# Performance work log

Measured on AMD Instinct MI355X. Metric: run time of the kernel, lower is better.

## Reference

```python
import jax, jax.numpy as jnp
import numpy as np

N_CHANNELS = 22
N_PATCHES = 64
N_NODES = N_CHANNELS * N_PATCHES  # 1408
EMBED_DIM = 256
N_HEADS = 4
HEAD_DIM = EMBED_DIM // N_HEADS
ALPHA = 0.15
TOP_P = 0.85
DIST_THRESH = 0.55
BATCH = 16

TCP_PAIRS = [('FP1','F7'),('F7','T3'),('T3','T5'),('T5','O1'),('FP2','F8'),('F8','T4'),('T4','T6'),('T6','O2'),('FP1','F3'),('F3','C3'),('C3','P3'),('P3','O1'),('FP2','F4'),('F4','C4'),('C4','P4'),('P4','O2'),('A1','T3'),('T3','C3'),('C3','CZ'),('CZ','C4'),('C4','T4'),('T4','A2')]
_ELECTRODE_3D = {'FP1':(-0.31,0.95,0.0),'FP2':(0.31,0.95,0.0),'F7':(-0.81,0.59,0.0),'F3':(-0.55,0.67,0.5),'FZ':(0.0,0.71,0.71),'F4':(0.55,0.67,0.5),'F8':(0.81,0.59,0.0),'T3':(-1.0,0.0,0.0),'C3':(-0.57,0.0,0.82),'CZ':(0.0,0.0,1.0),'C4':(0.57,0.0,0.82),'T4':(1.0,0.0,0.0),'T5':(-0.81,-0.59,0.0),'P3':(-0.55,-0.67,0.5),'PZ':(0.0,-0.71,0.71),'P4':(0.55,-0.67,0.5),'T6':(0.81,-0.59,0.0),'O1':(-0.31,-0.95,0.0),'O2':(0.31,-0.95,0.0),'A1':(-1.05,0.0,-0.3),'A2':(1.05,0.0,-0.3)}


def _build_masks():
    # channel positions = midpoint of each bipolar TCP pair -> [22,3]
    ch_pos = np.array([(np.array(_ELECTRODE_3D[a]) + np.array(_ELECTRODE_3D[b])) / 2.0 for a, b in TCP_PAIRS])
    d = np.linalg.norm(ch_pos[:, None, :] - ch_pos[None, :, :], axis=-1)
    ch_adj = (d < DIST_THRESH).astype(np.float32)
    np.fill_diagonal(ch_adj, 0.0)
    # node = ch * n_patches + t ; spatial edges only between same t: kron(ch_adj, I_P)
    spatial = np.kron(ch_adj, np.eye(N_PATCHES, dtype=np.float32))
    # temporal: same channel, |p - p'| == 1
    T = np.zeros((N_PATCHES, N_PATCHES), dtype=np.float32)
    idx = np.arange(N_PATCHES - 1)
    T[idx, idx + 1] = 1.0
    T[idx + 1, idx] = 1.0
    temporal = np.kron(np.eye(N_CHANNELS, dtype=np.float32), T)
    return jnp.asarray(temporal), jnp.asarray(spatial)


def setup_inputs() -> dict:
    key = jax.random.key(0)
    ks = jax.random.split(key, 8)
    D, H, HD = EMBED_DIM, N_HEADS, HEAD_DIM
    s = 1.0 / np.sqrt(D)
    x = jax.random.normal(ks[0], (BATCH, N_NODES, D), dtype=jnp.float32)
    proj_w = jax.random.uniform(ks[1], (H, HD, D), jnp.float32, -s, s)
    gate_w = jax.random.uniform(ks[2], (3, D), jnp.float32, -s, s)
    gate_b = jax.random.uniform(ks[3], (3,), jnp.float32, -s, s)
    score_w1 = jax.random.uniform(ks[4], (D // 2, D), jnp.float32, -s, s)
    score_b1 = jax.random.uniform(ks[5], (D // 2,), jnp.float32, -s, s)
    s2 = 1.0 / np.sqrt(D // 2)
    score_w2 = jax.random.uniform(ks[6], (1, D // 2), jnp.float32, -s2, s2)
    score_b2 = jax.random.uniform(ks[7], (1,), jnp.float32, -s2, s2)
    threshold = jnp.asarray(0.5, dtype=jnp.float32)
    temporal_mask, spatial_mask = _build_masks()
    return {"x": x, "proj_w": proj_w, "gate_w": gate_w, "gate_b": gate_b,
            "score_w1": score_w1, "score_b1": score_b1, "score_w2": score_w2,
            "score_b2": score_b2, "threshold": threshold,
            "temporal_mask": temporal_mask, "spatial_mask": spatial_mask}


def _safe_dist(d2):
    d2 = jnp.maximum(d2, 0.0)
    return jnp.where(d2 > 0, jnp.sqrt(jnp.where(d2 > 0, d2, 1.0)), 0.0)


def reference(x, proj_w, gate_w, gate_b, score_w1, score_b1, score_w2, score_b2,
              threshold, temporal_mask, spatial_mask):
    B, N, D = x.shape
    H = proj_w.shape[0]
    k = max(1, int(N * ALPHA))
    b_idx = jnp.arange(B)[:, None, None]
    r_idx = jnp.arange(N)[None, :, None]

    # ---- MultiHeadDistanceKNN: mean over heads of (knn-mask * gaussian sim) ----
    adj = jnp.zeros((B, N, N), x.dtype)
    for h in range(H):
        z = x @ proj_w[h].T                                  # [B,N,hd]
        sq = jnp.sum(z * z, axis=-1)                         # [B,N]
        d2 = sq[:, :, None] + sq[:, None, :] - 2.0 * jnp.einsum('bnd,bmd->bnm', z, z)
        dist = _safe_dist(d2)                                # [B,N,N]
        _, topk_idx = jax.lax.top_k(-dist, k)                # k smallest dists
        m = jnp.zeros((B, N, N), x.dtype).at[b_idx, r_idx, topk_idx].set(1.0)
        m = jnp.maximum(m, jnp.swapaxes(m, -1, -2))          # symmetrize
        sim = jnp.exp(-dist * dist / (2.0 * jnp.mean(dist) ** 2 + 1e-8))
        adj = adj + sim * m
    adj = adj / H

    # ---- Temporal / Spatial filters (fixed masks) ----
    adj_t = adj * temporal_mask[None]
    adj_s = adj * spatial_mask[None]

    # ---- Pathological filter: MLP node score -> outer product -> soft gate ----
    h1 = jax.nn.gelu(x @ score_w1.T + score_b1, approximate=False)
    scores = jax.nn.sigmoid((h1 @ score_w2.T + score_b2)[..., 0])    # [B,N]
    edge_w = scores[:, :, None] * scores[:, None, :]
    adj_p = adj * jax.nn.sigmoid((edge_w - threshold) * 10.0)

    # ---- NoisyGatedRouter (eval: no noise): softmax -> top-p truncate -> renorm ----
    probs = jax.nn.softmax(x @ gate_w.T + gate_b, axis=-1)           # [B,N,3]
    order = jnp.argsort(-probs, axis=-1)
    sp = jnp.take_along_axis(probs, order, axis=-1)
    keep = (jnp.cumsum(sp, axis=-1) - sp) < TOP_P
    sp = sp * keep.astype(sp.dtype)
    inv = jnp.argsort(order, axis=-1)
    w = jnp.take_along_axis(sp, inv, axis=-1)                        # scatter back
    w = w / (jnp.sum(w, axis=-1, keepdims=True) + 1e-8)              # [B,N,3]

    # ---- Mix filters with per-edge weights (w_i + w_j)/2 ----
    out = jnp.zeros_like(adj)
    for f, a in enumerate((adj_t, adj_s, adj_p)):
        wf = w[:, :, f]
        ewf = (wf[:, :, None] + wf[:, None, :]) * 0.5
        out = out + a * ewf
    return out
```

## Files before the change

### kernel.cpp

```cpp
#include <hip/hip_runtime.h>
#include <math.h>

typedef __attribute__((ext_vector_type(8))) short bf16x8;
typedef __attribute__((ext_vector_type(4))) float f32x4;

__device__ __forceinline__ float wsum64(float v) {
#pragma unroll
  for (int d = 32; d > 0; d >>= 1) v += __shfl_xor(v, d, 64);
  return v;
}

__device__ __forceinline__ unsigned short f2bf(float f) {
  unsigned u = __float_as_uint(f);
  u = (u + 0x7FFFu + ((u >> 16) & 1u)) >> 16;
  return (unsigned short)u;
}

__global__ void k_init(const float* __restrict__ smask, float* __restrict__ chadj,
                       double* __restrict__ sums) {
  int t = threadIdx.x;
  if (t < 4) sums[t] = 0.0;
  if (t < 484) {
    int c1 = t / 22, c2 = t % 22;
    chadj[t] = smask[(size_t)(c1 * 64) * 1408 + (size_t)c2 * 64];
  }
}

__global__ __launch_bounds__(256) void k_gemm_in(
    const float* __restrict__ x, const float* __restrict__ projw,
    const float* __restrict__ w1, float* __restrict__ z, float* __restrict__ zT,
    unsigned short* __restrict__ zb, float* __restrict__ h1) {
  __shared__ float xs[16][68];
  __shared__ float wsT[16][68];
  __shared__ float ldsT[64][65];
  int n0 = blockIdx.x * 64;
  int o0 = blockIdx.y * 64;
  int tid = threadIdx.x;
  int tx = tid & 15, ty = tid >> 4;
  float acc[4][4];
#pragma unroll
  for (int i = 0; i < 4; i++)
#pragma unroll
    for (int j = 0; j < 4; j++) acc[i][j] = 0.f;
  for (int kc = 0; kc < 16; kc++) {
#pragma unroll
    for (int rep = 0; rep < 4; rep++) {
      int e = tid + rep * 256;
      int n = e >> 4, k = e & 15;
      xs[k][n] = x[(size_t)(n0 + n) * 256 + kc * 16 + k];
      int row = o0 + n;
      wsT[k][n] = (row < 256) ? projw[(size_t)row * 256 + kc * 16 + k]
                              : w1[(size_t)(row - 256) * 256 + kc * 16 + k];
    }
    __syncthreads();
#pragma unroll
    for (int k = 0; k < 16; k++) {
      float4 a4 = *(const float4*)&xs[k][4 * ty];
      float4 w4 = *(const float4*)&wsT[k][4 * tx];
      float ar[4] = {a4.x, a4.y, a4.z, a4.w};
      float wr[4] = {w4.x, w4.y, w4.z, w4.w};
#pragma unroll
      for (int i = 0; i < 4; i++)
#pragma unroll
        for (int j = 0; j < 4; j++) acc[i][j] = fmaf(ar[i], wr[j], acc[i][j]);
    }
    __syncthreads();
  }
  if (blockIdx.y >= 4) {
#pragma unroll
    for (int i = 0; i < 4; i++) {
      size_t base = (size_t)(n0 + 4 * ty + i) * 128 + (o0 - 256) + 4 * tx;
      float4 t;
      t.x = acc[i][0]; t.y = acc[i][1]; t.z = acc[i][2]; t.w = acc[i][3];
      *(float4*)&h1[base] = t;
    }
  } else {
#pragma unroll
    for (int i = 0; i < 4; i++) {
      size_t base = (size_t)(n0 + 4 * ty + i) * 256 + o0 + 4 * tx;
      float4 t;
      t.x = acc[i][0]; t.y = acc[i][1]; t.z = acc[i][2]; t.w = acc[i][3];
      *(float4*)&z[base] = t;
      unsigned lo = (unsigned)f2bf(acc[i][0]) | ((unsigned)f2bf(acc[i][1]) << 16);
      unsigned hi = (unsigned)f2bf(acc[i][2]) | ((unsigned)f2bf(acc[i][3]) << 16);
      uint2 u2; u2.x = lo; u2.y = hi;
      *(uint2*)(zb + base) = u2;
    }
    __syncthreads();
#pragma unroll
    for (int i = 0; i < 4; i++)
#pragma unroll
      for (int j = 0; j < 4; j++) ldsT[4 * tx + j][4 * ty + i] = acc[i][j];
    __syncthreads();
    int bblk = blockIdx.x / 22;
    int nbase = (blockIdx.x % 22) * 64;
#pragma unroll
    for (int rep = 0; rep < 16; rep++) {
      int e = tid + rep * 256;
      int oo = e >> 6, nn = e & 63;
      zT[(size_t)((bblk * 4 + blockIdx.y) * 64 + oo) * 1408 + nbase + nn] = ldsT[oo][nn];
    }
  }
}

__global__ __launch_bounds__(256) void k_node(
    const float* __restrict__ x, const float* __restrict__ z,
    const float* __restrict__ h1, const float* __restrict__ gw,
    const float* __restrict__ gb, const float* __restrict__ b1,
    const float* __restrict__ w2, const float* __restrict__ b2v,
    float* __restrict__ sq, float4* __restrict__ wnode) {
  int tid = threadIdx.x;
  int w = tid >> 6, lane = tid & 63;
  int node = blockIdx.x * 4 + w;
  int b = node / 1408, n = node % 1408;
  const float* zr = z + (size_t)node * 256;
  const float* xr = x + (size_t)node * 256;
#pragma unroll
  for (int c = 0; c < 4; c++) {
    float val = zr[c * 64 + lane];
    float s = wsum64(val * val);
    if (lane == 0) sq[(size_t)(b * 4 + c) * 1408 + n] = s;
  }
  float gl[3];
#pragma unroll
  for (int f = 0; f < 3; f++) {
    float p = 0.f;
#pragma unroll
    for (int c = 0; c < 4; c++)
      p = fmaf(xr[c * 64 + lane], gw[f * 256 + c * 64 + lane], p);
    gl[f] = wsum64(p) + gb[f];
  }
  const float* hr = h1 + (size_t)node * 128;
  float ps = 0.f;
#pragma unroll
  for (int c = 0; c < 2; c++) {
    float t = hr[c * 64 + lane] + b1[c * 64 + lane];
    float g = 0.5f * t * (1.f + erff(t * 0.7071067811865475f));
    ps = fmaf(g, w2[c * 64 + lane], ps);
  }
  float sc = wsum64(ps) + b2v[0];
  sc = 1.f / (1.f + expf(-sc));
  float mx = fmaxf(gl[0], fmaxf(gl[1], gl[2]));
  float ex[3];
  float esum = 0.f;
#pragma unroll
  for (int f = 0; f < 3; f++) { ex[f] = expf(gl[f] - mx); esum += ex[f]; }
  float p3[3];
#pragma unroll
  for (int f = 0; f < 3; f++) p3[f] = ex[f] / esum;
  int rk[3];
#pragma unroll
  for (int f = 0; f < 3; f++) {
    int r = 0;
#pragma unroll
    for (int g = 0; g < 3; g++)
      r += ((p3[g] > p3[f]) || (p3[g] == p3[f] && g < f)) ? 1 : 0;
    rk[f] = r;
  }
  float sp[3]; int oi[3];
#pragma unroll
  for (int f = 0; f < 3; f++) { sp[rk[f]] = p3[f]; oi[rk[f]] = f; }
  bool k1 = sp[0] < 0.85f;
  bool k2 = (sp[0] + sp[1]) < 0.85f;
  float wv[3];
  wv[oi[0]] = sp[0];
  wv[oi[1]] = k1 ? sp[1] : 0.f;
  wv[oi[2]] = k2 ? sp[2] : 0.f;
  float inv = 1.f / (wv[0] + wv[1] + wv[2] + 1e-8f);
  if (lane == 0) wnode[node] = make_float4(wv[0] * inv, wv[1] * inv, wv[2] * inv, sc);
}

__global__ __launch_bounds__(256, 2) void k_pass1(
    const float* __restrict__ zT, const float* __restrict__ sq,
    unsigned* __restrict__ bm, double* __restrict__ sums) {
  __shared__ float As[64][16];
  __shared__ float srowL[16];
  __shared__ unsigned hist[4][2112];
  __shared__ float cand[4][64];
  __shared__ unsigned candCnt[4];
  __shared__ int tbinS[4], rstarS[4];
  __shared__ float TS[4];
  int b = blockIdx.y, h = blockIdx.z;
  int i0 = blockIdx.x * 16;
  int tid = threadIdx.x;
  int w = tid >> 6, lane = tid & 63;
  const float* zTh = zT + (size_t)((b * 4 + h) * 64) * 1408;
  const float* sqh = sq + (size_t)(b * 4 + h) * 1408;
#pragma unroll
  for (int rep = 0; rep < 4; rep++) {
    int e = tid + rep * 256;
    int k = e >> 4, r = e & 15;
    As[k][r] = zTh[(size_t)k * 1408 + i0 + r];
  }
  if (tid < 16) srowL[tid] = sqh[i0 + tid];
  const int tc = (w < 2) ? 6 : 5;
  const float* bp[6];
  float sqj[6];
#pragma unroll
  for (int t = 0; t < 6; t++) {
    int jb = (w + 4 * t) * 64 + lane;
    bp[t] = zTh + ((t < tc) ? jb : lane);
    sqj[t] = (t < tc) ? sqh[jb] : 0.f;
  }
  float v[16][6];
#pragma unroll
  for (int r = 0; r < 16; r++)
#pragma unroll
    for (int t = 0; t < 6; t++) v[r][t] = 0.f;
  __syncthreads();
  float bc[6];
#pragma unroll
  for (int t = 0; t < 6; t++) bc[t] = bp[t][0];
  for (int k = 0; k < 64; k++) {
    float bn[6];
    if (k < 63) {
#pragma unroll
      for (int t = 0; t < 6; t++) bn[t] = bp[t][(size_t)(k + 1) * 1408];
    }
    float4 a0 = *(const float4*)&As[k][0];
    float4 a1 = *(const float4*)&As[k][4];
    float4 a2 = *(const float4*)&As[k][8];
    float4 a3 = *(const float4*)&As[k][12];
    float ar[16] = {a0.x, a0.y, a0.z, a0.w, a1.x, a1.y, a1.z, a1.w,
                    a2.x, a2.y, a2.z, a2.w, a3.x, a3.y, a3.z, a3.w};
#pragma unroll
    for (int r = 0; r < 16; r++)
#pragma unroll
      for (int t = 0; t < 6; t++) v[r][t] = fmaf(ar[r], bc[t], v[r][t]);
#pragma unroll
    for (int t = 0; t < 6; t++) bc[t] = bn[t];
  }
  float ssum = 0.f;
#pragma unroll
  for (int r = 0; r < 16; r++) {
    float sr = srowL[r];
#pragma unroll
    for (int t = 0; t < 6; t++) {
      float d = sr + sqj[t] - 2.f * v[r][t];
      d = fmaxf(d, 0.f);
      bool vld = (t < tc);
      if (vld) ssum += sqrtf(d);
      v[r][t] = vld ? d : INFINITY;
    }
  }
  unsigned* histF = &hist[0][0];
#pragma unroll
  for (int g = 0; g < 4; g++) {
#pragma unroll
    for (int u = 0; u < 33; u++) histF[u * 256 + tid] = 0u;
    if (tid < 4) candCnt[tid] = 0u;
    __syncthreads();
#pragma unroll
    for (int rr = 0; rr < 4; rr++) {
#pragma unroll
      for (int t = 0; t < 6; t++) {
        if (t < tc) {
          float val = v[g * 4 + rr][t];
          unsigned key = (unsigned)fminf(val * 16.0f, 2047.0f);
          atomicAdd(&hist[rr][key + (key >> 5)], 1u);
        }
      }
    }
    __syncthreads();
    {
      int rr = w;
      unsigned ssb = 0;
      int sbase = 33 * lane;
#pragma unroll
      for (int t = 0; t < 32; t++) ssb += hist[rr][sbase + t];
      unsigned inc = ssb;
#pragma unroll
      for (int d = 1; d < 64; d <<= 1) {
        unsigned u = __shfl_up(inc, d, 64);
        if (lane >= d) inc += u;
      }
      unsigned long long mk = __ballot(inc >= 211u);
      int Ls = __ffsll(mk) - 1;
      unsigned cbefore = (Ls > 0) ? (unsigned)__shfl((int)inc, Ls - 1, 64) : 0u;
      unsigned v2 = (lane < 32) ? hist[rr][33 * Ls + lane] : 0u;
      unsigned inc2 = v2;
#pragma unroll
      for (int d = 1; d < 32; d <<= 1) {
        unsigned u = __shfl_up(inc2, d, 64);
        if (lane >= d) inc2 += u;
      }
      bool c2 = (lane < 32) && (cbefore + inc2 >= 211u);
      mk = __ballot(c2);
      int is = __ffsll(mk) - 1;
      unsigned cbelow = cbefore + ((is > 0) ? (unsigned)__shfl((int)inc2, is - 1, 64) : 0u);
      if (lane == 0) {
        tbinS[rr] = Ls * 32 + is;
        rstarS[rr] = 211 - (int)cbelow;
      }
    }
    __syncthreads();
#pragma unroll
    for (int rr = 0; rr < 4; rr++) {
      int tb = tbinS[rr];
#pragma unroll
      for (int t = 0; t < 6; t++) {
        if (t < tc) {
          float val = v[g * 4 + rr][t];
          unsigned key = (unsigned)fminf(val * 16.0f, 2047.0f);
          if ((int)key == tb) {
            unsigned id = atomicAdd(&candCnt[rr], 1u);
            if (id < 64u) cand[rr][id] = val;
          }
        }
      }
    }
    __syncthreads();
    {
      int rr = w;
      int rstar = rstarS[rr];
      unsigned craw = candCnt[rr];
      int cnt = (craw > 64u) ? 64 : (int)craw;
      float t2l = INFINITY;
      if (lane < cnt) {
        float xm = cand[rr][lane];
        int below = 0, eq = 0;
        for (int m = 0; m < cnt; m++) {
          float y = cand[rr][m];
          below += (y < xm) ? 1 : 0;
          eq += (y == xm) ? 1 : 0;
        }
        if (below < rstar && rstar <= below + eq) t2l = xm;
      }
#pragma unroll
      for (int dd = 32; dd > 0; dd >>= 1) t2l = fminf(t2l, __shfl_xor(t2l, dd, 64));
      if (lane == 0) TS[rr] = t2l;
    }
    __syncthreads();
#pragma unroll
    for (int rr = 0; rr < 4; rr++) {
      float T = TS[rr];
      int row = i0 + g * 4 + rr;
      unsigned* bmrow = bm + (size_t)((h * 16 + b) * 1408 + row) * 44;
#pragma unroll
      for (int t = 0; t < 6; t++) {
        if (t < tc) {
          unsigned long long bl = __ballot(v[g * 4 + rr][t] <= T);
          int tile = w + 4 * t;
          if (lane == 0) bmrow[tile * 2] = (unsigned)bl;
          if (lane == 32) bmrow[tile * 2 + 1] = (unsigned)(bl >> 32);
        }
      }
    }
    __syncthreads();
  }
  ssum = wsum64(ssum);
  if (lane == 0) atomicAdd(&sums[h], (double)ssum);
}

__global__ __launch_bounds__(256) void k_final(
    const unsigned short* __restrict__ zb, const float* __restrict__ sq,
    const float4* __restrict__ wnode, const unsigned* __restrict__ bm,
    const double* __restrict__ sums, const float* __restrict__ chadj,
    const float* __restrict__ thrp, float* __restrict__ out) {
  int it = blockIdx.x, jt = blockIdx.y, b = blockIdx.z;
  int tid = threadIdx.x, wv = tid >> 6, lane = tid & 63;
  int quad = lane >> 4, l15 = lane & 15;
  float c2h[4];
#pragma unroll
  for (int h = 0; h < 4; h++) {
    double mu = sums[h] * (1.0 / (16.0 * 1408.0 * 1408.0));
    c2h[h] = (float)(1.0 / (2.0 * mu * mu + 1e-8)) * 1.44269504088896f;
  }
  float thr = thrp[0];
  int ib = it * 64 + wv * 16;
  const unsigned short* za = zb + (size_t)(b * 1408 + ib + l15) * 256;
  bf16x8 af[4][2];
#pragma unroll
  for (int h = 0; h < 4; h++)
#pragma unroll
    for (int k0 = 0; k0 < 2; k0++)
      af[h][k0] = *(const bf16x8*)(za + h * 64 + k0 * 32 + quad * 8);
  int ibq = ib + quad * 4;
  float4 wi[4];
  float sqi[4][4];
#pragma unroll
  for (int reg = 0; reg < 4; reg++) {
    int i = ibq + reg;
    wi[reg] = wnode[b * 1408 + i];
#pragma unroll
    for (int h = 0; h < 4; h++) sqi[reg][h] = sq[(size_t)(b * 4 + h) * 1408 + i];
  }
#pragma unroll
  for (int js = 0; js < 4; js++) {
    int j = jt * 64 + js * 16 + l15;
    const unsigned short* zj = zb + (size_t)(b * 1408 + j) * 256;
    f32x4 acc[4];
#pragma unroll
    for (int h = 0; h < 4; h++) {
      bf16x8 b0 = *(const bf16x8*)(zj + h * 64 + quad * 8);
      bf16x8 b1f = *(const bf16x8*)(zj + h * 64 + 32 + quad * 8);
      f32x4 a = {0.f, 0.f, 0.f, 0.f};
      a = __builtin_amdgcn_mfma_f32_16x16x32_bf16(af[h][0], b0, a, 0, 0, 0);
      a = __builtin_amdgcn_mfma_f32_16x16x32_bf16(af[h][1], b1f, a, 0, 0, 0);
      acc[h] = a;
    }
    float sqj[4];
#pragma unroll
    for (int h = 0; h < 4; h++) sqj[h] = sq[(size_t)(b * 4 + h) * 1408 + j];
    float4 wj = wnode[b * 1408 + j];
    float adjv[4] = {0.f, 0.f, 0.f, 0.f};
#pragma unroll
    for (int h = 0; h < 4; h++) {
      const unsigned* bmh = bm + (size_t)(h * 16 + b) * 1408 * 44;
      unsigned wJ = bmh[(size_t)j * 44 + (ibq >> 5)];
#pragma unroll
      for (int reg = 0; reg < 4; reg++) {
        int i = ibq + reg;
        float d2 = sqi[reg][h] + sqj[h] - 2.f * acc[h][reg];
        d2 = fmaxf(d2, 0.f);
        float sim = exp2f(-d2 * c2h[h]);
        unsigned bi = bmh[(size_t)i * 44 + (j >> 5)] >> (j & 31);
        unsigned bj = wJ >> (i & 31);
        adjv[reg] += (((bi | bj) & 1u) != 0u) ? sim : 0.f;
      }
    }
#pragma unroll
    for (int reg = 0; reg < 4; reg++) {
      int i = ibq + reg;
      int chi = i >> 6, pi = i & 63, chj = j >> 6, pj = j & 63;
      float e0 = 0.5f * (wi[reg].x + wj.x);
      float e1 = 0.5f * (wi[reg].y + wj.y);
      float e2 = 0.5f * (wi[reg].z + wj.z);
      float a2 = 0.f;
      if (chi == chj) {
        int dp = pi - pj;
        if (dp == 1 || dp == -1) a2 += e0;
      }
      if (pi == pj && chadj[chi * 22 + chj] != 0.f) a2 += e1;
      float xw = (wi[reg].w * wj.w - thr) * 10.f;
      float pt = 1.f / (1.f + exp2f(-xw * 1.44269504088896f));
      a2 += pt * e2;
      out[(size_t)(b * 1408 + i) * 1408 + j] = 0.25f * adjv[reg] * a2;
    }
  }
}

extern "C" void kernel_launch(void* const* d_in, const int* in_sizes, int n_in,
                              void* d_out, int out_size, void* d_ws, size_t ws_size,
                              hipStream_t stream) {
  (void)in_sizes; (void)n_in; (void)out_size; (void)ws_size;
  const float* x = (const float*)d_in[0];
  const float* projw = (const float*)d_in[1];
  const float* gw = (const float*)d_in[2];
  const float* gb = (const float*)d_in[3];
  const float* w1 = (const float*)d_in[4];
  const float* b1 = (const float*)d_in[5];
  const float* w2 = (const float*)d_in[6];
  const float* b2 = (const float*)d_in[7];
  const float* thr = (const float*)d_in[8];
  const float* smask = (const float*)d_in[10];
  float* out = (float*)d_out;
  char* ws = (char*)d_ws;
  size_t off = 0;
  auto take = [&](size_t bytes) {
    char* p = ws + off;
    off += (bytes + 255) & ~(size_t)255;
    return p;
  };
  float* z = (float*)take((size_t)22528 * 256 * 4);
  float* zT = (float*)take((size_t)22528 * 256 * 4);
  unsigned short* zb = (unsigned short*)take((size_t)22528 * 256 * 2);
  float* h1 = (float*)take((size_t)22528 * 128 * 4);
  float* sq = (float*)take((size_t)16 * 4 * 1408 * 4);
  float4* wnode = (float4*)take((size_t)22528 * 16);
  unsigned* bm = (unsigned*)take((size_t)4 * 16 * 1408 * 44 * 4);
  float* chadj = (float*)take(484 * 4);
  double* sums = (double*)take(4 * 8);

  hipLaunchKernelGGL(k_init, dim3(1), dim3(512), 0, stream, smask, chadj, sums);
  hipLaunchKernelGGL(k_gemm_in, dim3(352, 6), dim3(256), 0, stream, x, projw, w1,
                     z, zT, zb, h1);
  hipLaunchKernelGGL(k_node, dim3(5632), dim3(256), 0, stream, x, z, h1, gw, gb,
                     b1, w2, b2, sq, wnode);
  hipLaunchKernelGGL(k_pass1, dim3(88, 16, 4), dim3(256), 0, stream, zT, sq, bm,
                     sums);
  hipLaunchKernelGGL(k_final, dim3(22, 22, 16), dim3(256), 0, stream, zb, sq,
                     wnode, bm, sums, chadj, thr, out);
}
```

Measured before the change: 1.037 ms.

## Restructure pass1 top-k selection into a single-pass packed histogram over all rows

Replaces the four-round per-group histogram and threshold selection in k_pass1 with a single pass. It builds a coarser 512-bin histogram for all 16 rows at once, packing two rows into each 32-bit counter as 16-bit halves, with larger candidate buffers. The distance dot-product loop is templated on the per-wave tile count with contiguous tiles per wave, and launch bounds are raised to 3 blocks per CU. This removes many barriers and halves shared memory to allow more resident blocks, at the cost of more candidates per threshold bin and possible register pressure under the tighter occupancy target.

```diff
diff --git a/kernel.cpp b/kernel.cpp
--- a/kernel.cpp
+++ b/kernel.cpp
@@ -170,16 +170,62 @@
   if (lane == 0) wnode[node] = make_float4(wv[0] * inv, wv[1] * inv, wv[2] * inv, sc);
 }
 
-__global__ __launch_bounds__(256, 2) void k_pass1(
+template <int TC>
+__device__ __forceinline__ void dotstrip16(float (&v)[16][6],
+                                           const float* __restrict__ zTh,
+                                           const float (&As)[64][16], int jb) {
+#pragma unroll
+  for (int r = 0; r < 16; r++)
+#pragma unroll
+    for (int t = 0; t < TC; t++) v[r][t] = 0.f;
+  const float* bp = zTh + jb;
+  float bc[TC];
+#pragma unroll
+  for (int t = 0; t < TC; t++) bc[t] = bp[t * 64];
+  const float* pn = bp + 1408;
+#pragma unroll 1
+  for (int k = 0; k < 63; k++) {
+    float bn[TC];
+#pragma unroll
+    for (int t = 0; t < TC; t++) bn[t] = pn[t * 64];
+    pn += 1408;
+    float4 a0 = *(const float4*)&As[k][0];
+    float4 a1 = *(const float4*)&As[k][4];
+    float4 a2 = *(const float4*)&As[k][8];
+    float4 a3 = *(const float4*)&As[k][12];
+    float ar[16] = {a0.x, a0.y, a0.z, a0.w, a1.x, a1.y, a1.z, a1.w,
+                    a2.x, a2.y, a2.z, a2.w, a3.x, a3.y, a3.z, a3.w};
+#pragma unroll
+    for (int r = 0; r < 16; r++)
+#pragma unroll
+      for (int t = 0; t < TC; t++) v[r][t] = fmaf(ar[r], bc[t], v[r][t]);
+#pragma unroll
+    for (int t = 0; t < TC; t++) bc[t] = bn[t];
+  }
+  {
+    float4 a0 = *(const float4*)&As[63][0];
+    float4 a1 = *(const float4*)&As[63][4];
+    float4 a2 = *(const float4*)&As[63][8];
+    float4 a3 = *(const float4*)&As[63][12];
+    float ar[16] = {a0.x, a0.y, a0.z, a0.w, a1.x, a1.y, a1.z, a1.w,
+                    a2.x, a2.y, a2.z, a2.w, a3.x, a3.y, a3.z, a3.w};
+#pragma unroll
+    for (int r = 0; r < 16; r++)
+#pragma unroll
+      for (int t = 0; t < TC; t++) v[r][t] = fmaf(ar[r], bc[t], v[r][t]);
+  }
+}
+
+__global__ __launch_bounds__(256, 3) void k_pass1(
     const float* __restrict__ zT, const float* __restrict__ sq,
     unsigned* __restrict__ bm, double* __restrict__ sums) {
   __shared__ float As[64][16];
   __shared__ float srowL[16];
-  __shared__ unsigned hist[4][2112];
-  __shared__ float cand[4][64];
-  __shared__ unsigned candCnt[4];
-  __shared__ int tbinS[4], rstarS[4];
-  __shared__ float TS[4];
+  __shared__ unsigned hist[8][528];
+  __shared__ float cand[16][128];
+  __shared__ unsigned candCnt[16];
+  __shared__ int tbinS[16], rstarS[16];
+  __shared__ float TS[16];
   int b = blockIdx.y, h = blockIdx.z;
   int i0 = blockIdx.x * 16;
   int tid = threadIdx.x;
@@ -193,160 +239,134 @@
     As[k][r] = zTh[(size_t)k * 1408 + i0 + r];
   }
   if (tid < 16) srowL[tid] = sqh[i0 + tid];
-  const int tc = (w < 2) ? 6 : 5;
-  const float* bp[6];
+  {
+    unsigned* histF = &hist[0][0];
+    for (int u = tid; u < 8 * 528; u += 256) histF[u] = 0u;
+  }
+  if (tid < 16) candCnt[tid] = 0u;
+  __syncthreads();
+
+  const int TC = (w < 2) ? 6 : 5;
+  const int tbase = (w < 2) ? 6 * w : 5 * w + 2;
+  int jb = tbase * 64 + lane;
   float sqj[6];
 #pragma unroll
-  for (int t = 0; t < 6; t++) {
-    int jb = (w + 4 * t) * 64 + lane;
-    bp[t] = zTh + ((t < tc) ? jb : lane);
-    sqj[t] = (t < tc) ? sqh[jb] : 0.f;
-  }
+  for (int t = 0; t < 6; t++)
+    sqj[t] = (t < 5 || TC == 6) ? sqh[jb + t * 64] : 0.f;
+
   float v[16][6];
-#pragma unroll
-  for (int r = 0; r < 16; r++)
-#pragma unroll
-    for (int t = 0; t < 6; t++) v[r][t] = 0.f;
-  __syncthreads();
-  float bc[6];
-#pragma unroll
-  for (int t = 0; t < 6; t++) bc[t] = bp[t][0];
-  for (int k = 0; k < 64; k++) {
-    float bn[6];
-    if (k < 63) {
-#pragma unroll
-      for (int t = 0; t < 6; t++) bn[t] = bp[t][(size_t)(k + 1) * 1408];
-    }
-    float4 a0 = *(const float4*)&As[k][0];
-    float4 a1 = *(const float4*)&As[k][4];
-    float4 a2 = *(const float4*)&As[k][8];
-    float4 a3 = *(const float4*)&As[k][12];
-    float ar[16] = {a0.x, a0.y, a0.z, a0.w, a1.x, a1.y, a1.z, a1.w,
-                    a2.x, a2.y, a2.z, a2.w, a3.x, a3.y, a3.z, a3.w};
-#pragma unroll
-    for (int r = 0; r < 16; r++)
-#pragma unroll
-      for (int t = 0; t < 6; t++) v[r][t] = fmaf(ar[r], bc[t], v[r][t]);
-#pragma unroll
-    for (int t = 0; t < 6; t++) bc[t] = bn[t];
-  }
+  if (w < 2) dotstrip16<6>(v, zTh, As, jb);
+  else       dotstrip16<5>(v, zTh, As, jb);
+
   float ssum = 0.f;
 #pragma unroll
   for (int r = 0; r < 16; r++) {
     float sr = srowL[r];
 #pragma unroll
     for (int t = 0; t < 6; t++) {
-      float d = sr + sqj[t] - 2.f * v[r][t];
-      d = fmaxf(d, 0.f);
-      bool vld = (t < tc);
-      if (vld) ssum += sqrtf(d);
-      v[r][t] = vld ? d : INFINITY;
-    }
-  }
-  unsigned* histF = &hist[0][0];
-#pragma unroll
-  for (int g = 0; g < 4; g++) {
-#pragma unroll
-    for (int u = 0; u < 33; u++) histF[u * 256 + tid] = 0u;
-    if (tid < 4) candCnt[tid] = 0u;
-    __syncthreads();
-#pragma unroll
-    for (int rr = 0; rr < 4; rr++) {
-#pragma unroll
-      for (int t = 0; t < 6; t++) {
-        if (t < tc) {
-          float val = v[g * 4 + rr][t];
-          unsigned key = (unsigned)fminf(val * 16.0f, 2047.0f);
-          atomicAdd(&hist[rr][key + (key >> 5)], 1u);
+      if (t < 5 || TC == 6) {
+        float d = sr + sqj[t] - 2.f * v[r][t];
+        d = fmaxf(d, 0.f);
+        ssum += sqrtf(d);
+        v[r][t] = d;
+        unsigned key = (unsigned)fminf(d * 4.0f, 511.0f);
+        atomicAdd(&hist[r >> 1][key + (key >> 6)], 1u << ((r & 1) * 16));
+      }
+    }
+  }
+  __syncthreads();
+
+#pragma unroll 1
+  for (int q = 0; q < 4; q++) {
+    int r = 4 * w + q;
+    int sh = (r & 1) * 16;
+    const unsigned* hrow = hist[r >> 1];
+    unsigned partial = 0;
+#pragma unroll
+    for (int u = 0; u < 8; u++) {
+      int bin = 8 * lane + u;
+      partial += (hrow[bin + (bin >> 6)] >> sh) & 0xffffu;
+    }
+    unsigned inc = partial;
+#pragma unroll
+    for (int d = 1; d < 64; d <<= 1) {
+      unsigned u2 = __shfl_up(inc, d, 64);
+      if (lane >= d) inc += u2;
+    }
+    unsigned long long mk = __ballot(inc >= 211u);
+    int Ls = __ffsll(mk) - 1;
+    unsigned cbefore = (Ls > 0) ? (unsigned)__shfl((int)inc, Ls - 1, 64) : 0u;
+    int tb = -1;
+    unsigned run = cbefore, cbelow = cbefore;
+#pragma unroll
+    for (int u = 0; u < 8; u++) {
+      int bin = 8 * Ls + u;
+      unsigned c = (hrow[bin + (bin >> 6)] >> sh) & 0xffffu;
+      if (tb < 0) {
+        if (run + c >= 211u) { tb = bin; cbelow = run; }
+        run += c;
+      }
+    }
+    if (lane == 0) { tbinS[r] = tb; rstarS[r] = 211 - (int)cbelow; }
+  }
+  __syncthreads();
+
+#pragma unroll
+  for (int r = 0; r < 16; r++) {
+    int tb = tbinS[r];
+#pragma unroll
+    for (int t = 0; t < 6; t++) {
+      if (t < 5 || TC == 6) {
+        float d = v[r][t];
+        unsigned key = (unsigned)fminf(d * 4.0f, 511.0f);
+        if ((int)key == tb) {
+          unsigned id = atomicAdd(&candCnt[r], 1u);
+          if (id < 128u) cand[r][id] = d;
         }
       }
     }
-    __syncthreads();
-    {
-      int rr = w;
-      unsigned ssb = 0;
-      int sbase = 33 * lane;
-#pragma unroll
-      for (int t = 0; t < 32; t++) ssb += hist[rr][sbase + t];
-      unsigned inc = ssb;
-#pragma unroll
-      for (int d = 1; d < 64; d <<= 1) {
-        unsigned u = __shfl_up(inc, d, 64);
-        if (lane >= d) inc += u;
-      }
-      unsigned long long mk = __ballot(inc >= 211u);
-      int Ls = __ffsll(mk) - 1;
-      unsigned cbefore = (Ls > 0) ? (unsigned)__shfl((int)inc, Ls - 1, 64) : 0u;
-      unsigned v2 = (lane < 32) ? hist[rr][33 * Ls + lane] : 0u;
-      unsigned inc2 = v2;
-#pragma unroll
-      for (int d = 1; d < 32; d <<= 1) {
-        unsigned u = __shfl_up(inc2, d, 64);
-        if (lane >= d) inc2 += u;
-      }
-      bool c2 = (lane < 32) && (cbefore + inc2 >= 211u);
-      mk = __ballot(c2);
-      int is = __ffsll(mk) - 1;
-      unsigned cbelow = cbefore + ((is > 0) ? (unsigned)__shfl((int)inc2, is - 1, 64) : 0u);
-      if (lane == 0) {
-        tbinS[rr] = Ls * 32 + is;
-        rstarS[rr] = 211 - (int)cbelow;
-      }
-    }
-    __syncthreads();
-#pragma unroll
-    for (int rr = 0; rr < 4; rr++) {
-      int tb = tbinS[rr];
-#pragma unroll
-      for (int t = 0; t < 6; t++) {
-        if (t < tc) {
-          float val = v[g * 4 + rr][t];
-          unsigned key = (unsigned)fminf(val * 16.0f, 2047.0f);
-          if ((int)key == tb) {
-            unsigned id = atomicAdd(&candCnt[rr], 1u);
-            if (id < 64u) cand[rr][id] = val;
-          }
-        }
-      }
-    }
-    __syncthreads();
-    {
-      int rr = w;
-      int rstar = rstarS[rr];
-      unsigned craw = candCnt[rr];
-      int cnt = (craw > 64u) ? 64 : (int)craw;
-      float t2l = INFINITY;
-      if (lane < cnt) {
-        float xm = cand[rr][lane];
+  }
+  __syncthreads();
+
+#pragma unroll 1
+  for (int q = 0; q < 4; q++) {
+    int r = 4 * w + q;
+    int rstar = rstarS[r];
+    unsigned craw = candCnt[r];
+    int cnt = (craw > 128u) ? 128 : (int)craw;
+    float t2l = INFINITY;
+    for (int base = 0; base < cnt; base += 64) {
+      int ci = base + lane;
+      if (ci < cnt) {
+        float xm = cand[r][ci];
         int below = 0, eq = 0;
         for (int m = 0; m < cnt; m++) {
-          float y = cand[rr][m];
+          float y = cand[r][m];
           below += (y < xm) ? 1 : 0;
           eq += (y == xm) ? 1 : 0;
         }
-        if (below < rstar && rstar <= below + eq) t2l = xm;
-      }
-#pragma unroll
-      for (int dd = 32; dd > 0; dd >>= 1) t2l = fminf(t2l, __shfl_xor(t2l, dd, 64));
-      if (lane == 0) TS[rr] = t2l;
-    }
-    __syncthreads();
-#pragma unroll
-    for (int rr = 0; rr < 4; rr++) {
-      float T = TS[rr];
-      int row = i0 + g * 4 + rr;
-      unsigned* bmrow = bm + (size_t)((h * 16 + b) * 1408 + row) * 44;
-#pragma unroll
-      for (int t = 0; t < 6; t++) {
-        if (t < tc) {
-          unsigned long long bl = __ballot(v[g * 4 + rr][t] <= T);
-          int tile = w + 4 * t;
-          if (lane == 0) bmrow[tile * 2] = (unsigned)bl;
-          if (lane == 32) bmrow[tile * 2 + 1] = (unsigned)(bl >> 32);
-        }
-      }
-    }
-    __syncthreads();
+        if (below < rstar && rstar <= below + eq) t2l = fminf(t2l, xm);
+      }
+    }
+#pragma unroll
+    for (int dd = 32; dd > 0; dd >>= 1) t2l = fminf(t2l, __shfl_xor(t2l, dd, 64));
+    if (lane == 0) TS[r] = t2l;
+  }
+  __syncthreads();
+
+#pragma unroll
+  for (int r = 0; r < 16; r++) {
+    float T = TS[r];
+    unsigned* bmrow = bm + (size_t)((h * 16 + b) * 1408 + i0 + r) * 44;
+#pragma unroll
+    for (int t = 0; t < 6; t++) {
+      if (t < 5 || TC == 6) {
+        unsigned long long bl = __ballot(v[r][t] <= T);
+        int tile = tbase + t;
+        if (lane == 0) bmrow[tile * 2] = (unsigned)bl;
+        if (lane == 32) bmrow[tile * 2 + 1] = (unsigned)(bl >> 32);
+      }
+    }
   }
   ssum = wsum64(ssum);
   if (lane == 0) atomicAdd(&sums[h], (double)ssum);
```

Result: faster. 917.4 us (-11.6%).
